# Kernel optimization log

Measured on AMD Instinct MI355X. Metric: run time of the kernel, lower is better.

Reference implementation:

```python
import jax, jax.numpy as jnp
import numpy as np

N_DATES, M_FACTORS, N_SIMS = 252, 8, 65536

def setup_inputs() -> dict:
    key = jax.random.key(0)
    k1, k2, k3 = jax.random.split(key, 3)
    cov = jax.random.normal(k1, (N_DATES, M_FACTORS, M_FACTORS), dtype=jnp.float32) * 0.1
    var = jax.random.uniform(k2, (N_DATES, M_FACTORS), dtype=jnp.float32) * 0.04
    z = jax.random.normal(k3, (N_DATES, M_FACTORS, N_SIMS), dtype=jnp.float32)
    return {"cov": cov, "var": var, "z": z}

def reference(cov, var, z):
    # per-date factor shock: dW[i] = cov[i] @ z[i] - var[i]/2  (broadcast over sims)
    dW = jnp.einsum('nij,njs->nis', cov, z) - var[:, :, None] * 0.5
    # running log-sample accumulation over dates (sampleValues[date_i] = sum_{k<=i} dW[k])
    logsamples = jnp.cumsum(dW, axis=0)  # [n_dates, m, n_sims]
    return logsamples
```

## Files before the change

kernel.cpp:

```cpp
#include <hip/hip_runtime.h>

#define N_DATES 252
#define M_FACTORS 8
#define N_SIMS 65536

__global__ __launch_bounds__(64)
void evo_lognormal_kernel(const float* __restrict__ cov,
                          const float* __restrict__ var,
                          const float* __restrict__ z,
                          float* __restrict__ out) {
    const int s = blockIdx.x * 64 + threadIdx.x;
    const float* zp = z + s;
    float* op = out + s;

    float acc[M_FACTORS];
#pragma unroll
    for (int i = 0; i < M_FACTORS; ++i) acc[i] = 0.0f;

    float bufA[M_FACTORS];
    float bufB[M_FACTORS];

#pragma unroll
    for (int j = 0; j < M_FACTORS; ++j)
        bufA[j] = zp[(size_t)j * N_SIMS];

    for (int n = 0; n < N_DATES; n += 2) {
        {
            const float* znext = zp + (size_t)(n + 1) * M_FACTORS * N_SIMS;
#pragma unroll
            for (int j = 0; j < M_FACTORS; ++j)
                bufB[j] = znext[(size_t)j * N_SIMS];
        }

        {
            const float* covn = cov + (size_t)n * (M_FACTORS * M_FACTORS);
            const float* varn = var + (size_t)n * M_FACTORS;
            float* on = op + (size_t)n * M_FACTORS * N_SIMS;
#pragma unroll
            for (int i = 0; i < M_FACTORS; ++i) {
                float d = -0.5f * varn[i];
#pragma unroll
                for (int j = 0; j < M_FACTORS; ++j)
                    d = fmaf(covn[i * M_FACTORS + j], bufA[j], d);
                acc[i] += d;
                on[(size_t)i * N_SIMS] = acc[i];
            }
        }

        if (n + 2 < N_DATES) {
            const float* znext = zp + (size_t)(n + 2) * M_FACTORS * N_SIMS;
#pragma unroll
            for (int j = 0; j < M_FACTORS; ++j)
                bufA[j] = znext[(size_t)j * N_SIMS];
        }

        {
            const int n1 = n + 1;
            const float* covn = cov + (size_t)n1 * (M_FACTORS * M_FACTORS);
            const float* varn = var + (size_t)n1 * M_FACTORS;
            float* on = op + (size_t)n1 * M_FACTORS * N_SIMS;
#pragma unroll
            for (int i = 0; i < M_FACTORS; ++i) {
                float d = -0.5f * varn[i];
#pragma unroll
                for (int j = 0; j < M_FACTORS; ++j)
                    d = fmaf(covn[i * M_FACTORS + j], bufB[j], d);
                acc[i] += d;
                on[(size_t)i * N_SIMS] = acc[i];
            }
        }
    }
}

extern "C" void kernel_launch(void* const* d_in, const int* in_sizes, int n_in,
                              void* d_out, int out_size, void* d_ws, size_t ws_size,
                              hipStream_t stream) {
    const float* cov = (const float*)d_in[0];
    const float* var = (const float*)d_in[1];
    const float* z   = (const float*)d_in[2];
    float* out = (float*)d_out;

    dim3 block(64);
    dim3 grid(N_SIMS / 64);
    evo_lognormal_kernel<<<grid, block, 0, stream>>>(cov, var, z, out);
}
```

Measured before the change: 1.061 ms.

## Split date scan into chunked three-pass scan with float2 sims per thread

Replaces the single sequential-over-dates kernel with a three-kernel chunked scan. Pass one computes per-chunk totals over 12 chunks of 21 dates, pass two does an exclusive scan across chunks, and pass three recomputes each chunk and writes outputs. Each thread also handles two simulations through float2 loads and stores. This exposes more parallelism than the original 1024 blocks of 64 threads, at the cost of reading z twice plus workspace traffic and two extra launches.

New measurement: 1.061 ms. No clear change (-0.0%).

```diff
diff --git a/kernel.cpp b/kernel.cpp
--- a/kernel.cpp
+++ b/kernel.cpp
@@ -3,72 +3,131 @@
 #define N_DATES 252
 #define M_FACTORS 8
 #define N_SIMS 65536
+#define SIMS2 (N_SIMS / 2)
+#define CHUNKS 12
+#define DPC 21
+#define BLK 256
+#define BLOCKS_PER_CHUNK (SIMS2 / BLK)
 
-__global__ __launch_bounds__(64)
-void evo_lognormal_kernel(const float* __restrict__ cov,
-                          const float* __restrict__ var,
-                          const float* __restrict__ z,
-                          float* __restrict__ out) {
-    const int s = blockIdx.x * 64 + threadIdx.x;
-    const float* zp = z + s;
-    float* op = out + s;
+__device__ __forceinline__
+void date_body(const float* __restrict__ cov, const float* __restrict__ var,
+               int n, const float2 (&buf)[M_FACTORS], float2 (&acc)[M_FACTORS]) {
+    const float* covn = cov + (size_t)n * (M_FACTORS * M_FACTORS);
+    const float* varn = var + (size_t)n * M_FACTORS;
+#pragma unroll
+    for (int i = 0; i < M_FACTORS; ++i) {
+        float dx = -0.5f * varn[i];
+        float dy = dx;
+#pragma unroll
+        for (int j = 0; j < M_FACTORS; ++j) {
+            const float w = covn[i * M_FACTORS + j];
+            dx = fmaf(w, buf[j].x, dx);
+            dy = fmaf(w, buf[j].y, dy);
+        }
+        acc[i].x += dx;
+        acc[i].y += dy;
+    }
+}
 
-    float acc[M_FACTORS];
+__device__ __forceinline__
+void load_date(const float2* __restrict__ z2, int n, int s2, float2 (&buf)[M_FACTORS]) {
+    const size_t base = ((size_t)n * M_FACTORS) * SIMS2 + s2;
 #pragma unroll
-    for (int i = 0; i < M_FACTORS; ++i) acc[i] = 0.0f;
+    for (int j = 0; j < M_FACTORS; ++j)
+        buf[j] = z2[base + (size_t)j * SIMS2];
+}
 
-    float bufA[M_FACTORS];
-    float bufB[M_FACTORS];
+__global__ __launch_bounds__(BLK)
+void k1_chunk_totals(const float* __restrict__ cov,
+                     const float* __restrict__ var,
+                     const float2* __restrict__ z2,
+                     float2* __restrict__ totals2) {
+    const int c = blockIdx.x / BLOCKS_PER_CHUNK;
+    const int lb = blockIdx.x % BLOCKS_PER_CHUNK;
+    const int s2 = lb * BLK + threadIdx.x;
+    const int n0 = c * DPC;
+
+    float2 acc[M_FACTORS];
+#pragma unroll
+    for (int i = 0; i < M_FACTORS; ++i) acc[i] = make_float2(0.f, 0.f);
+
+    float2 bufA[M_FACTORS], bufB[M_FACTORS];
+    load_date(z2, n0, s2, bufA);
 
 #pragma unroll
-    for (int j = 0; j < M_FACTORS; ++j)
-        bufA[j] = zp[(size_t)j * N_SIMS];
+    for (int p = 0; p < (DPC - 1) / 2; ++p) {
+        const int n = n0 + 2 * p;
+        load_date(z2, n + 1, s2, bufB);
+        date_body(cov, var, n, bufA, acc);
+        load_date(z2, n + 2, s2, bufA);
+        date_body(cov, var, n + 1, bufB, acc);
+    }
+    date_body(cov, var, n0 + DPC - 1, bufA, acc);
 
-    for (int n = 0; n < N_DATES; n += 2) {
+#pragma unroll
+    for (int i = 0; i < M_FACTORS; ++i)
+        totals2[((size_t)c * M_FACTORS + i) * SIMS2 + s2] = acc[i];
+}
+
+__global__ __launch_bounds__(BLK)
+void k2_scan(float2* __restrict__ totals2) {
+    const int t = blockIdx.x * BLK + threadIdx.x;
+    const int i = t / SIMS2;
+    const int s2 = t % SIMS2;
+    float2 run = make_float2(0.f, 0.f);
+#pragma unroll
+    for (int c = 0; c < CHUNKS; ++c) {
+        const size_t idx = ((size_t)c * M_FACTORS + i) * SIMS2 + s2;
+        float2 v = totals2[idx];
+        totals2[idx] = run;
+        run.x += v.x;
+        run.y += v.y;
+    }
+}
+
+__global__ __launch_bounds__(BLK)
+void k3_emit(const float* __restrict__ cov,
+             const float* __restrict__ var,
+             const float2* __restrict__ z2,
+             const float2* __restrict__ totals2,
+             float2* __restrict__ out2) {
+    const int c = blockIdx.x / BLOCKS_PER_CHUNK;
+    const int lb = blockIdx.x % BLOCKS_PER_CHUNK;
+    const int s2 = lb * BLK + threadIdx.x;
+    const int n0 = c * DPC;
+
+    float2 acc[M_FACTORS];
+#pragma unroll
+    for (int i = 0; i < M_FACTORS; ++i)
+        acc[i] = totals2[((size_t)c * M_FACTORS + i) * SIMS2 + s2];
+
+    float2 bufA[M_FACTORS], bufB[M_FACTORS];
+    load_date(z2, n0, s2, bufA);
+
+#pragma unroll
+    for (int p = 0; p < (DPC - 1) / 2; ++p) {
+        const int n = n0 + 2 * p;
+        load_date(z2, n + 1, s2, bufB);
+        date_body(cov, var, n, bufA, acc);
         {
-            const float* znext = zp + (size_t)(n + 1) * M_FACTORS * N_SIMS;
+            float2* on = out2 + ((size_t)n * M_FACTORS) * SIMS2 + s2;
 #pragma unroll
-            for (int j = 0; j < M_FACTORS; ++j)
-                bufB[j] = znext[(size_t)j * N_SIMS];
+            for (int i = 0; i < M_FACTORS; ++i) on[(size_t)i * SIMS2] = acc[i];
         }
-
+        load_date(z2, n + 2, s2, bufA);
+        date_body(cov, var, n + 1, bufB, acc);
         {
-            const float* covn = cov + (size_t)n * (M_FACTORS * M_FACTORS);
-            const float* varn = var + (size_t)n * M_FACTORS;
-            float* on = op + (size_t)n * M_FACTORS * N_SIMS;
+            float2* on = out2 + ((size_t)(n + 1) * M_FACTORS) * SIMS2 + s2;
 #pragma unroll
-            for (int i = 0; i < M_FACTORS; ++i) {
-                float d = -0.5f * varn[i];
+            for (int i = 0; i < M_FACTORS; ++i) on[(size_t)i * SIMS2] = acc[i];
+        }
+    }
+    {
+        const int n = n0 + DPC - 1;
+        date_body(cov, var, n, bufA, acc);
+        float2* on = out2 + ((size_t)n * M_FACTORS) * SIMS2 + s2;
 #pragma unroll
-                for (int j = 0; j < M_FACTORS; ++j)
-                    d = fmaf(covn[i * M_FACTORS + j], bufA[j], d);
-                acc[i] += d;
-                on[(size_t)i * N_SIMS] = acc[i];
-            }
-        }
-
-        if (n + 2 < N_DATES) {
-            const float* znext = zp + (size_t)(n + 2) * M_FACTORS * N_SIMS;
-#pragma unroll
-            for (int j = 0; j < M_FACTORS; ++j)
-                bufA[j] = znext[(size_t)j * N_SIMS];
-        }
-
-        {
-            const int n1 = n + 1;
-            const float* covn = cov + (size_t)n1 * (M_FACTORS * M_FACTORS);
-            const float* varn = var + (size_t)n1 * M_FACTORS;
-            float* on = op + (size_t)n1 * M_FACTORS * N_SIMS;
-#pragma unroll
-            for (int i = 0; i < M_FACTORS; ++i) {
-                float d = -0.5f * varn[i];
-#pragma unroll
-                for (int j = 0; j < M_FACTORS; ++j)
-                    d = fmaf(covn[i * M_FACTORS + j], bufB[j], d);
-                acc[i] += d;
-                on[(size_t)i * N_SIMS] = acc[i];
-            }
-        }
+        for (int i = 0; i < M_FACTORS; ++i) on[(size_t)i * SIMS2] = acc[i];
     }
 }
 
@@ -77,10 +136,12 @@
                               hipStream_t stream) {
     const float* cov = (const float*)d_in[0];
     const float* var = (const float*)d_in[1];
-    const float* z   = (const float*)d_in[2];
-    float* out = (float*)d_out;
+    const float2* z2 = (const float2*)d_in[2];
+    float2* out2 = (float2*)d_out;
+    float2* totals2 = (float2*)d_ws;
 
-    dim3 block(64);
-    dim3 grid(N_SIMS / 64);
-    evo_lognormal_kernel<<<grid, block, 0, stream>>>(cov, var, z, out);
+    dim3 blk(BLK);
+    k1_chunk_totals<<<dim3(CHUNKS * BLOCKS_PER_CHUNK), blk, 0, stream>>>(cov, var, z2, totals2);
+    k2_scan<<<dim3((M_FACTORS * SIMS2) / BLK), blk, 0, stream>>>(totals2);
+    k3_emit<<<dim3(CHUNKS * BLOCKS_PER_CHUNK), blk, 0, stream>>>(cov, var, z2, totals2, out2);
 }
```
